# Optimization experiments

Measured on AMD Instinct MI355X. Metric: run time of the kernel, lower is better.

## Reference

```python
import jax, jax.numpy as jnp
import numpy as np

D_MODEL = 4096
N_HEADS = 32
HEAD_DIM = 128
MAX_SEQ = 512


def setup_inputs() -> dict:
    key = jax.random.key(0)
    ks = jax.random.split(key, 14)
    w_scale = 1.0 / np.sqrt(D_MODEL)
    inp = {
        "query": jax.random.normal(ks[0], (1, 1, D_MODEL), jnp.float32),
        "key_value_source": jax.random.normal(ks[1], (1, 1, D_MODEL), jnp.float32),
        "step": jax.random.randint(ks[2], (1,), 0, MAX_SEQ, jnp.int32),
        "key_buffer": jax.random.normal(ks[3], (1, N_HEADS, MAX_SEQ, HEAD_DIM), jnp.float32),
        "value_buffer": jax.random.normal(ks[4], (1, N_HEADS, MAX_SEQ, HEAD_DIM), jnp.float32),
        "Wq": jax.random.normal(ks[5], (D_MODEL, D_MODEL), jnp.float32) * w_scale,
        "bq": jax.random.normal(ks[6], (D_MODEL,), jnp.float32) * 0.01,
        "Wk": jax.random.normal(ks[7], (D_MODEL, D_MODEL), jnp.float32) * w_scale,
        "bk": jax.random.normal(ks[8], (D_MODEL,), jnp.float32) * 0.01,
        "Wv": jax.random.normal(ks[9], (D_MODEL, D_MODEL), jnp.float32) * w_scale,
        "bv": jax.random.normal(ks[10], (D_MODEL,), jnp.float32) * 0.01,
        "Wo": jax.random.normal(ks[11], (D_MODEL, D_MODEL), jnp.float32) * w_scale,
        "bo": jax.random.normal(ks[12], (D_MODEL,), jnp.float32) * 0.01,
    }
    return inp


def reference(query, key_value_source, step, key_buffer, value_buffer,
              Wq, bq, Wk, bk, Wv, bv, Wo, bo):
    # q/k/v projections on the single new token: [1,1,D] -> [1,H,1,HD]
    q = (query @ Wq.T + bq).reshape(1, 1, N_HEADS, HEAD_DIM).transpose(0, 2, 1, 3)
    k_new = (key_value_source @ Wk.T + bk).reshape(1, 1, N_HEADS, HEAD_DIM).transpose(0, 2, 1, 3)
    v_new = (key_value_source @ Wv.T + bv).reshape(1, 1, N_HEADS, HEAD_DIM).transpose(0, 2, 1, 3)

    positions = jnp.arange(MAX_SEQ)                       # [S]
    write_mask = (positions == step)[None, None, :, None]  # [1,1,S,1]
    key_buffer = jnp.where(write_mask, k_new, key_buffer)     # scatter-write at step
    value_buffer = jnp.where(write_mask, v_new, value_buffer)

    scale = 1.0 / np.sqrt(HEAD_DIM)
    attn_mask = jnp.where(positions <= step, 0.0, -jnp.inf)[None, None, None, :]  # [1,1,1,S]
    scores = jnp.einsum("bhqd,bhsd->bhqs", q, key_buffer) * scale + attn_mask
    weights = jax.nn.softmax(scores, axis=-1)
    attn_out = jnp.einsum("bhqs,bhsd->bhqd", weights, value_buffer)  # [1,H,1,HD]

    attn_out = attn_out.transpose(0, 2, 1, 3).reshape(1, 1, D_MODEL)
    output = attn_out @ Wo.T + bo
    return output, key_buffer, value_buffer
```

## Files before the change

kernel.cpp:

```cpp
#include <hip/hip_runtime.h>

#define D_MODEL 4096
#define N_HEADS 32
#define HEAD_DIM 128
#define MAX_SEQ 512
#define SPLITS 8
#define SPLIT_LEN (MAX_SEQ / SPLITS)

__global__ void qkv_gemv(const float* __restrict__ Wq, const float* __restrict__ bq,
                         const float* __restrict__ Wk, const float* __restrict__ bk,
                         const float* __restrict__ Wv, const float* __restrict__ bv,
                         const float* __restrict__ query, const float* __restrict__ kvsrc,
                         float* __restrict__ qkv_out) {
    const int wid  = (blockIdx.x * blockDim.x + threadIdx.x) >> 6;
    const int lane = threadIdx.x & 63;
    const int which = wid >> 12;
    const int row   = wid & (D_MODEL - 1);

    const float* W = (which == 0) ? Wq : (which == 1) ? Wk : Wv;
    const float* b = (which == 0) ? bq : (which == 1) ? bk : bv;
    const float* x = (which == 0) ? query : kvsrc;

    const float4* W4 = (const float4*)(W + (size_t)row * D_MODEL);
    const float4* x4 = (const float4*)x;

    float acc = 0.f;
#pragma unroll
    for (int j = 0; j < D_MODEL / 4; j += 64) {
        float4 w = W4[j + lane];
        float4 v = x4[j + lane];
        acc += w.x * v.x + w.y * v.y + w.z * v.z + w.w * v.w;
    }
#pragma unroll
    for (int off = 32; off > 0; off >>= 1) acc += __shfl_xor(acc, off);
    if (lane == 0) qkv_out[wid] = acc + b[row];
}

__global__ void kv_update(const float4* __restrict__ kb, const float4* __restrict__ vb,
                          const float4* __restrict__ knew, const float4* __restrict__ vnew,
                          const int* __restrict__ step_p,
                          float4* __restrict__ out_kb, float4* __restrict__ out_vb) {
    const int step = *step_p;
    const int n4 = N_HEADS * MAX_SEQ * HEAD_DIM / 4;
    for (int i = blockIdx.x * blockDim.x + threadIdx.x; i < n4; i += gridDim.x * blockDim.x) {
        const int s  = (i >> 5) & (MAX_SEQ - 1);
        const int h  = i >> 14;
        const int d4 = i & 31;
        if (s == step) {
            out_kb[i] = knew[h * 32 + d4];
            out_vb[i] = vnew[h * 32 + d4];
        } else {
            out_kb[i] = kb[i];
            out_vb[i] = vb[i];
        }
    }
}

__global__ void attn_split(const float* __restrict__ q,
                           const float* __restrict__ kb,
                           const float* __restrict__ vb,
                           const int* __restrict__ step_p,
                           float* __restrict__ pm, float* __restrict__ pl,
                           float* __restrict__ po) {
    const int bid = blockIdx.x;
    const int h   = bid >> 3;
    const int sp  = bid & (SPLITS - 1);
    const int tid = threadIdx.x;
    const int n   = *step_p + 1;
    const int s0  = sp * SPLIT_LEN;
    const int cnt = min(SPLIT_LEN, n - s0);

    if (cnt <= 0) {
        if (tid == 0) { pm[bid] = -1e30f; pl[bid] = 0.f; }
        if (tid < HEAD_DIM) po[bid * HEAD_DIM + tid] = 0.f;
        return;
    }

    __shared__ float sq[HEAD_DIM];
    __shared__ float w[SPLIT_LEN];
    __shared__ float pv[2][HEAD_DIM];

    if (tid < HEAD_DIM) sq[tid] = q[h * HEAD_DIM + tid];
    __syncthreads();

    {
        const int p = tid >> 2;
        const int g = tid & 3;
        float acc = 0.f;
        if (p < cnt) {
            const float4* krow = (const float4*)(kb + ((size_t)(h * MAX_SEQ + s0 + p)) * HEAD_DIM);
            const float4* q4   = (const float4*)sq;
#pragma unroll
            for (int j = 0; j < 8; ++j) {
                float4 kk = krow[g * 8 + j];
                float4 qq = q4[g * 8 + j];
                acc += kk.x * qq.x + kk.y * qq.y + kk.z * qq.z + kk.w * qq.w;
            }
        }
        acc += __shfl_xor(acc, 1);
        acc += __shfl_xor(acc, 2);
        if ((g == 0) && (p < cnt)) w[p] = acc * 0.08838834764831845f;
    }
    __syncthreads();

    if (tid < 64) {
        float mv = (tid < cnt) ? w[tid] : -1e30f;
#pragma unroll
        for (int off = 32; off > 0; off >>= 1) mv = fmaxf(mv, __shfl_xor(mv, off));
        float e = (tid < cnt) ? __expf(w[tid] - mv) : 0.f;
        if (tid < cnt) w[tid] = e;
        float sum = e;
#pragma unroll
        for (int off = 32; off > 0; off >>= 1) sum += __shfl_xor(sum, off);
        if (tid == 0) { pm[bid] = mv; pl[bid] = sum; }
    }
    __syncthreads();

    const int d    = tid & (HEAD_DIM - 1);
    const int half = tid >> 7;
    float acc = 0.f;
    for (int s = half; s < cnt; s += 2)
        acc += w[s] * vb[((size_t)(h * MAX_SEQ + s0 + s)) * HEAD_DIM + d];
    pv[half][d] = acc;
    __syncthreads();
    if (tid < HEAD_DIM)
        po[bid * HEAD_DIM + tid] = pv[0][tid] + pv[1][tid];
}

__global__ void attn_combine(const float* __restrict__ pm, const float* __restrict__ pl,
                             const float* __restrict__ po, float* __restrict__ attn_out) {
    const int h = blockIdx.x;
    const int d = threadIdx.x;
    float m = -1e30f;
#pragma unroll
    for (int j = 0; j < SPLITS; ++j) m = fmaxf(m, pm[h * SPLITS + j]);
    float l = 0.f, o = 0.f;
#pragma unroll
    for (int j = 0; j < SPLITS; ++j) {
        float sc = __expf(pm[h * SPLITS + j] - m);
        l += pl[h * SPLITS + j] * sc;
        o += po[(h * SPLITS + j) * HEAD_DIM + d] * sc;
    }
    attn_out[h * HEAD_DIM + d] = o / l;
}

__global__ void out_gemv(const float* __restrict__ Wo, const float* __restrict__ bo,
                         const float* __restrict__ x, float* __restrict__ out) {
    const int row  = (blockIdx.x * blockDim.x + threadIdx.x) >> 6;
    const int lane = threadIdx.x & 63;

    const float4* W4 = (const float4*)(Wo + (size_t)row * D_MODEL);
    const float4* x4 = (const float4*)x;

    float acc = 0.f;
#pragma unroll
    for (int j = 0; j < D_MODEL / 4; j += 64) {
        float4 w = W4[j + lane];
        float4 v = x4[j + lane];
        acc += w.x * v.x + w.y * v.y + w.z * v.z + w.w * v.w;
    }
#pragma unroll
    for (int off = 32; off > 0; off >>= 1) acc += __shfl_xor(acc, off);
    if (lane == 0) out[row] = acc + bo[row];
}

extern "C" void kernel_launch(void* const* d_in, const int* in_sizes, int n_in,
                              void* d_out, int out_size, void* d_ws, size_t ws_size,
                              hipStream_t stream) {
    const float* query  = (const float*)d_in[0];
    const float* kvsrc  = (const float*)d_in[1];
    const int*   step_p = (const int*)d_in[2];
    const float* kb     = (const float*)d_in[3];
    const float* vb     = (const float*)d_in[4];
    const float* Wq     = (const float*)d_in[5];
    const float* bq     = (const float*)d_in[6];
    const float* Wk     = (const float*)d_in[7];
    const float* bk     = (const float*)d_in[8];
    const float* Wv     = (const float*)d_in[9];
    const float* bv     = (const float*)d_in[10];
    const float* Wo     = (const float*)d_in[11];
    const float* bo     = (const float*)d_in[12];

    float* out    = (float*)d_out;
    float* out_kb = out + D_MODEL;
    float* out_vb = out_kb + N_HEADS * MAX_SEQ * HEAD_DIM;

    float* qkv  = (float*)d_ws;
    float* qv   = qkv;
    float* knew = qkv + D_MODEL;
    float* vnew = qkv + 2 * D_MODEL;
    float* attn = qkv + 3 * D_MODEL;
    float* pm   = attn + D_MODEL;
    float* pl   = pm + N_HEADS * SPLITS;
    float* po   = pl + N_HEADS * SPLITS;

    qkv_gemv<<<3 * D_MODEL / 4, 256, 0, stream>>>(Wq, bq, Wk, bk, Wv, bv, query, kvsrc, qkv);

    kv_update<<<2048, 256, 0, stream>>>((const float4*)kb, (const float4*)vb,
                                        (const float4*)knew, (const float4*)vnew,
                                        step_p, (float4*)out_kb, (float4*)out_vb);

    attn_split<<<N_HEADS * SPLITS, 256, 0, stream>>>(qv, out_kb, out_vb, step_p, pm, pl, po);
    attn_combine<<<N_HEADS, HEAD_DIM, 0, stream>>>(pm, pl, po, attn);

    out_gemv<<<D_MODEL / 4, 256, 0, stream>>>(Wo, bo, attn, out);
}
```

Baseline: 71.69 us.

## Fuse KV-row write into QKV GEMV, two rows per wave, split out GEMV

The QKV GEMV now computes two rows per wavefront, reusing each loaded x vector across both rows. It software-pipelines its loads two iterations ahead and writes the new K/V values straight into the output caches at the step position. kv_update then only copies rows other than the step row, with a fixed two-iteration loop over half as many blocks. The output GEMV splits each row across two waves, reduces through shared memory and prefetches similarly, doubling the blocks to raise parallelism. The aim is to cut the separate scatter reads, redundant x loads and latency stalls, but the copy and the fused write now race only in the sense of disjoint addresses, and correctness relies on that.

```diff
diff --git a/kernel.cpp b/kernel.cpp
--- a/kernel.cpp
+++ b/kernel.cpp
@@ -7,49 +7,72 @@
 #define SPLITS 8
 #define SPLIT_LEN (MAX_SEQ / SPLITS)
 
-__global__ void qkv_gemv(const float* __restrict__ Wq, const float* __restrict__ bq,
-                         const float* __restrict__ Wk, const float* __restrict__ bk,
-                         const float* __restrict__ Wv, const float* __restrict__ bv,
-                         const float* __restrict__ query, const float* __restrict__ kvsrc,
-                         float* __restrict__ qkv_out) {
+__global__ __launch_bounds__(256) void qkv_gemv(
+        const float* __restrict__ Wq, const float* __restrict__ bq,
+        const float* __restrict__ Wk, const float* __restrict__ bk,
+        const float* __restrict__ Wv, const float* __restrict__ bv,
+        const float* __restrict__ query, const float* __restrict__ kvsrc,
+        const int* __restrict__ step_p,
+        float* __restrict__ qkv_out,
+        float* __restrict__ out_kb, float* __restrict__ out_vb) {
     const int wid  = (blockIdx.x * blockDim.x + threadIdx.x) >> 6;
     const int lane = threadIdx.x & 63;
-    const int which = wid >> 12;
-    const int row   = wid & (D_MODEL - 1);
+    const int r0   = wid << 1;
+    const int which = r0 >> 12;
+    const int row   = r0 & (D_MODEL - 1);
 
     const float* W = (which == 0) ? Wq : (which == 1) ? Wk : Wv;
     const float* b = (which == 0) ? bq : (which == 1) ? bk : bv;
     const float* x = (which == 0) ? query : kvsrc;
 
-    const float4* W4 = (const float4*)(W + (size_t)row * D_MODEL);
-    const float4* x4 = (const float4*)x;
-
-    float acc = 0.f;
-#pragma unroll
-    for (int j = 0; j < D_MODEL / 4; j += 64) {
-        float4 w = W4[j + lane];
-        float4 v = x4[j + lane];
-        acc += w.x * v.x + w.y * v.y + w.z * v.z + w.w * v.w;
-    }
-#pragma unroll
-    for (int off = 32; off > 0; off >>= 1) acc += __shfl_xor(acc, off);
-    if (lane == 0) qkv_out[wid] = acc + b[row];
+    const float4* A = (const float4*)(W + (size_t)row * D_MODEL);
+    const float4* B = A + D_MODEL / 4;
+    const float4* X = (const float4*)x;
+
+    float4 a0 = A[lane],      b0 = B[lane],      x0 = X[lane];
+    float4 a1 = A[64 + lane], b1 = B[64 + lane], x1 = X[64 + lane];
+    float acc0 = 0.f, acc1 = 0.f;
+#pragma unroll
+    for (int j = 0; j < 16; ++j) {
+        float4 ac = a0, bc = b0, xc = x0;
+        a0 = a1; b0 = b1; x0 = x1;
+        if (j < 14) {
+            const int o = (j + 2) * 64 + lane;
+            a1 = A[o]; b1 = B[o]; x1 = X[o];
+        }
+        acc0 += ac.x * xc.x + ac.y * xc.y + ac.z * xc.z + ac.w * xc.w;
+        acc1 += bc.x * xc.x + bc.y * xc.y + bc.z * xc.z + bc.w * xc.w;
+    }
+#pragma unroll
+    for (int off = 32; off > 0; off >>= 1) {
+        acc0 += __shfl_xor(acc0, off);
+        acc1 += __shfl_xor(acc1, off);
+    }
+    if (lane == 0) {
+        const float v0 = acc0 + b[row];
+        const float v1 = acc1 + b[row + 1];
+        qkv_out[r0]     = v0;
+        qkv_out[r0 + 1] = v1;
+        if (which != 0) {
+            const int step = *step_p;
+            float* dst = (which == 1) ? out_kb : out_vb;
+            const int h0 = row >> 7, d0 = row & (HEAD_DIM - 1);
+            dst[((size_t)h0 * MAX_SEQ + step) * HEAD_DIM + d0]     = v0;
+            const int r1 = row + 1;
+            dst[((size_t)(r1 >> 7) * MAX_SEQ + step) * HEAD_DIM + (r1 & (HEAD_DIM - 1))] = v1;
+        }
+    }
 }
 
 __global__ void kv_update(const float4* __restrict__ kb, const float4* __restrict__ vb,
-                          const float4* __restrict__ knew, const float4* __restrict__ vnew,
                           const int* __restrict__ step_p,
                           float4* __restrict__ out_kb, float4* __restrict__ out_vb) {
     const int step = *step_p;
-    const int n4 = N_HEADS * MAX_SEQ * HEAD_DIM / 4;
-    for (int i = blockIdx.x * blockDim.x + threadIdx.x; i < n4; i += gridDim.x * blockDim.x) {
-        const int s  = (i >> 5) & (MAX_SEQ - 1);
-        const int h  = i >> 14;
-        const int d4 = i & 31;
-        if (s == step) {
-            out_kb[i] = knew[h * 32 + d4];
-            out_vb[i] = vnew[h * 32 + d4];
-        } else {
+    int i = blockIdx.x * blockDim.x + threadIdx.x;
+#pragma unroll
+    for (int t = 0; t < 2; ++t, i += 1024 * 256) {
+        const int s = (i >> 5) & (MAX_SEQ - 1);
+        if (s != step) {
             out_kb[i] = kb[i];
             out_vb[i] = vb[i];
         }
@@ -144,24 +167,40 @@
     attn_out[h * HEAD_DIM + d] = o / l;
 }
 
-__global__ void out_gemv(const float* __restrict__ Wo, const float* __restrict__ bo,
-                         const float* __restrict__ x, float* __restrict__ out) {
-    const int row  = (blockIdx.x * blockDim.x + threadIdx.x) >> 6;
+__global__ __launch_bounds__(256) void out_gemv(const float* __restrict__ Wo,
+                                                const float* __restrict__ bo,
+                                                const float* __restrict__ x,
+                                                float* __restrict__ out) {
+    __shared__ float r[4];
+    const int wv   = threadIdx.x >> 6;
     const int lane = threadIdx.x & 63;
-
-    const float4* W4 = (const float4*)(Wo + (size_t)row * D_MODEL);
-    const float4* x4 = (const float4*)x;
-
+    const int row  = (blockIdx.x << 1) + (wv >> 1);
+    const int half = wv & 1;
+
+    const float4* A = (const float4*)(Wo + (size_t)row * D_MODEL) + (half << 9);
+    const float4* X = (const float4*)x + (half << 9);
+
+    float4 a0 = A[lane], x0 = X[lane];
+    float4 a1 = A[64 + lane], x1 = X[64 + lane];
     float acc = 0.f;
 #pragma unroll
-    for (int j = 0; j < D_MODEL / 4; j += 64) {
-        float4 w = W4[j + lane];
-        float4 v = x4[j + lane];
-        acc += w.x * v.x + w.y * v.y + w.z * v.z + w.w * v.w;
+    for (int j = 0; j < 8; ++j) {
+        float4 ac = a0, xc = x0;
+        a0 = a1; x0 = x1;
+        if (j < 6) {
+            const int o = (j + 2) * 64 + lane;
+            a1 = A[o]; x1 = X[o];
+        }
+        acc += ac.x * xc.x + ac.y * xc.y + ac.z * xc.z + ac.w * xc.w;
     }
 #pragma unroll
     for (int off = 32; off > 0; off >>= 1) acc += __shfl_xor(acc, off);
-    if (lane == 0) out[row] = acc + bo[row];
+    if (lane == 0) r[wv] = acc;
+    __syncthreads();
+    if (threadIdx.x < 2) {
+        const int rr = (blockIdx.x << 1) + threadIdx.x;
+        out[rr] = r[threadIdx.x * 2] + r[threadIdx.x * 2 + 1] + bo[rr];
+    }
 }
 
 extern "C" void kernel_launch(void* const* d_in, const int* in_sizes, int n_in,
@@ -187,21 +226,19 @@
 
     float* qkv  = (float*)d_ws;
     float* qv   = qkv;
-    float* knew = qkv + D_MODEL;
-    float* vnew = qkv + 2 * D_MODEL;
     float* attn = qkv + 3 * D_MODEL;
     float* pm   = attn + D_MODEL;
     float* pl   = pm + N_HEADS * SPLITS;
     float* po   = pl + N_HEADS * SPLITS;
 
-    qkv_gemv<<<3 * D_MODEL / 4, 256, 0, stream>>>(Wq, bq, Wk, bk, Wv, bv, query, kvsrc, qkv);
-
-    kv_update<<<2048, 256, 0, stream>>>((const float4*)kb, (const float4*)vb,
-                                        (const float4*)knew, (const float4*)vnew,
+    qkv_gemv<<<1536, 256, 0, stream>>>(Wq, bq, Wk, bk, Wv, bv, query, kvsrc,
+                                       step_p, qkv, out_kb, out_vb);
+
+    kv_update<<<1024, 256, 0, stream>>>((const float4*)kb, (const float4*)vb,
                                         step_p, (float4*)out_kb, (float4*)out_vb);
 
     attn_split<<<N_HEADS * SPLITS, 256, 0, stream>>>(qv, out_kb, out_vb, step_p, pm, pl, po);
     attn_combine<<<N_HEADS, HEAD_DIM, 0, stream>>>(pm, pl, po, attn);
 
-    out_gemv<<<D_MODEL / 4, 256, 0, stream>>>(Wo, bo, attn, out);
-}
+    out_gemv<<<2048, 256, 0, stream>>>(Wo, bo, attn, out);
+}
```

Result: faster. 69.96 us (-2.4%).
